# Kernel tuning notes

Hardware: AMD Instinct MI355X
Metric: run time of the kernel (lower is better)

## Reference

```python
import jax, jax.numpy as jnp
import numpy as np

N = 50000      # nodes (B-rep faces)
E = 800000     # directed edges (avg degree 16)
F_IN = 9       # 8 surface-type flags + is_feature
H1, H2, C = 512, 128, 2


def setup_inputs() -> dict:
    key = jax.random.key(0)
    ks = jax.random.split(key, 8)
    x = jax.random.normal(ks[0], (N, F_IN), dtype=jnp.float32)
    edge_index = jax.random.randint(ks[1], (2, E), 0, N, dtype=jnp.int64)
    W1 = jax.random.normal(ks[2], (F_IN, H1), dtype=jnp.float32) / np.sqrt(F_IN)
    b1 = jnp.zeros((H1,), dtype=jnp.float32)
    W2 = jax.random.normal(ks[3], (H1, H2), dtype=jnp.float32) / np.sqrt(H1)
    b2 = jnp.zeros((H2,), dtype=jnp.float32)
    W3 = jax.random.normal(ks[4], (H2, C), dtype=jnp.float32) / np.sqrt(H2)
    b3 = jnp.zeros((C,), dtype=jnp.float32)
    return {"x": x, "W1": W1, "b1": b1, "W2": W2, "b2": b2,
            "W3": W3, "b3": b3, "edge_index": edge_index}


def reference(x, W1, b1, W2, b2, W3, b3, edge_index):
    n = x.shape[0]
    self_idx = jnp.arange(n, dtype=edge_index.dtype)
    # GCN with self-loops and symmetric normalization (PyG gcn_norm)
    src = jnp.concatenate([edge_index[0], self_idx])  # [E+N]
    dst = jnp.concatenate([edge_index[1], self_idx])  # [E+N]
    deg = jax.ops.segment_sum(jnp.ones_like(src, dtype=x.dtype), dst, num_segments=n)
    dinv = jnp.where(deg > 0, jax.lax.rsqrt(jnp.maximum(deg, 1.0)), 0.0)
    norm = dinv[src] * dinv[dst]  # [E+N]

    def gcn(h, W, b):
        h = h @ W                                   # [N, out]
        msg = h[src] * norm[:, None]                # gather + scale
        return jax.ops.segment_sum(msg, dst, num_segments=n) + b  # scatter-add

    h = jax.nn.relu(gcn(x, W1, b1))
    h = jax.nn.relu(gcn(h, W2, b2))
    # F.dropout with training=False is identity (inference mode)
    h = gcn(h, W3, b3)
    return jax.nn.log_softmax(h, axis=1)
```

## Files before the change

kernel.cpp:

```cpp
#include <hip/hip_runtime.h>
#include <hip/hip_bf16.h>

typedef __attribute__((ext_vector_type(8))) short short8;
typedef __attribute__((ext_vector_type(4))) float float4v;
typedef unsigned int uint;

#define NBLK 192

static __device__ __forceinline__ float2 up_bf2(uint v) {
    float2 r;
    r.x = __uint_as_float(v << 16);
    r.y = __uint_as_float(v & 0xffff0000u);
    return r;
}
static __device__ __forceinline__ short f2bf_bits(float x) {
    union { __hip_bfloat16 h; short s; } u;
    u.h = __float2bfloat16(x);
    return u.s;
}


__global__ __launch_bounds__(256) void k_hist(const int* __restrict__ dst, int E, int chunk,
        int shift, int nbuck, int* __restrict__ histBlk) {
    __shared__ int h[256];
    h[threadIdx.x] = 0;
    __syncthreads();
    int blk = blockIdx.x;
    int e0 = blk * chunk, e1 = min(E, e0 + chunk);
    for (int e = e0 + threadIdx.x; e < e1; e += 256)
        atomicAdd(&h[dst[e] >> shift], 1);
    __syncthreads();
    if (threadIdx.x < nbuck) histBlk[threadIdx.x * NBLK + blk] = h[threadIdx.x];
}


__global__ __launch_bounds__(256) void k_btot(const int* __restrict__ histBlk,
                                              int* __restrict__ btot) {
    __shared__ int s[256];
    int b = blockIdx.x, t = threadIdx.x;
    s[t] = (t < NBLK) ? histBlk[b * NBLK + t] : 0;
    __syncthreads();
    for (int off = 128; off; off >>= 1) {
        if (t < off) s[t] += s[t + off];
        __syncthreads();
    }
    if (t == 0) btot[b] = s[0];
}


__global__ __launch_bounds__(256) void k_bscan(const int* __restrict__ histBlk,
        const int* __restrict__ btot, int nbuck,
        int* __restrict__ baseBlk, int* __restrict__ bucketBase) {
    __shared__ int s[256], sb[256];
    int b = blockIdx.x, t = threadIdx.x;
    int v = (t < NBLK) ? histBlk[b * NBLK + t] : 0;
    s[t] = v;
    sb[t] = (t < nbuck) ? btot[t] : 0;
    __syncthreads();
    for (int off = 1; off < 256; off <<= 1) {
        int u = (t >= off) ? s[t - off] : 0;
        int u2 = (t >= off) ? sb[t - off] : 0;
        __syncthreads();
        s[t] += u;
        sb[t] += u2;
        __syncthreads();
    }
    int base = (b > 0) ? sb[b - 1] : 0;
    if (t < NBLK) baseBlk[b * NBLK + t] = base + s[t] - v;
    if (t == 0) bucketBase[b] = base;
}


__global__ __launch_bounds__(256) void k_scatterbin(const int* __restrict__ src,
        const int* __restrict__ dst, int E, int chunk, int shift, int nbuck,
        const int* __restrict__ baseBlk, uint* __restrict__ binned) {
    __shared__ int cur[256];
    int blk = blockIdx.x;
    if (threadIdx.x < nbuck) cur[threadIdx.x] = baseBlk[threadIdx.x * NBLK + blk];
    __syncthreads();
    int e0 = blk * chunk, e1 = min(E, e0 + chunk);
    int mask = (1 << shift) - 1;
    for (int e = e0 + threadIdx.x; e < e1; e += 256) {
        int d = dst[e];
        int pos = atomicAdd(&cur[d >> shift], 1);
        binned[pos] = (uint)src[e] | ((uint)(d & mask) << 24);
    }
}


__global__ __launch_bounds__(256) void k_csrbuild(const uint* __restrict__ binned,
        const int* __restrict__ bucketBase, const float* __restrict__ x,
        int E, int shift, int n, int nbuck,
        int* __restrict__ row_ptr, float* __restrict__ dinv, float* __restrict__ xs,
        int* __restrict__ csr) {
    __shared__ int cnt[256], lcur[256];
    int b = blockIdx.x, t = threadIdx.x;
    cnt[t] = 0;
    __syncthreads();
    int lo = bucketBase[b];
    int hi = (b + 1 < nbuck) ? bucketBase[b + 1] : E;
    for (int e = lo + t; e < hi; e += 256)
        atomicAdd(&cnt[binned[e] >> 24], 1);
    __syncthreads();
    int c = cnt[t];
    lcur[t] = c;
    __syncthreads();
    for (int off = 1; off < 256; off <<= 1) {
        int u = (t >= off) ? lcur[t - off] : 0;
        __syncthreads();
        lcur[t] += u;
        __syncthreads();
    }
    int node0 = b << shift;
    int nodeEnd = min(n, (b + 1) << shift);
    int cntNodes = nodeEnd - node0;
    int myBase = lo + lcur[t] - c;
    if (t < cntNodes) {
        row_ptr[node0 + t] = myBase;
        dinv[node0 + t] = rsqrtf((float)(c + 1));
    }
    if (b == nbuck - 1 && t == 0) row_ptr[n] = E;
    for (int j = t; j < cntNodes * 9; j += 256) {
        int nl = j / 9, f = j - nl * 9;
        float dnl = rsqrtf((float)(cnt[nl] + 1));
        xs[(size_t)(node0 + nl) * 9 + f] = dnl * x[(size_t)(node0 + nl) * 9 + f];
    }
    __syncthreads();
    lcur[t] = myBase;
    __syncthreads();
    for (int e = lo + t; e < hi; e += 256) {
        uint p = binned[e];
        int pos = atomicAdd(&lcur[p >> 24], 1);
        csr[pos] = (int)(p & 0xFFFFFF);
    }
}


__global__ __launch_bounds__(256) void k_agg1(const float* __restrict__ xs,
                       const float* __restrict__ dinv,
                       const int* __restrict__ row_ptr, const int* __restrict__ csr,
                       float* __restrict__ aggx, int n) {
    int node = blockIdx.x * 16 + (threadIdx.x >> 4);
    if (node >= n) return;
    int f = threadIdx.x & 15;
    bool act = f < 9;
    float acc = act ? xs[node * 9 + f] : 0.f;
    int e0 = row_ptr[node], e1 = row_ptr[node + 1];
    int e = e0;
    for (; e + 4 <= e1; e += 4) {
        int s0 = csr[e], s1 = csr[e + 1], s2 = csr[e + 2], s3 = csr[e + 3];
        float x0 = act ? xs[s0 * 9 + f] : 0.f;
        float x1 = act ? xs[s1 * 9 + f] : 0.f;
        float x2 = act ? xs[s2 * 9 + f] : 0.f;
        float x3 = act ? xs[s3 * 9 + f] : 0.f;
        acc += (x0 + x1) + (x2 + x3);
    }
    for (; e < e1; ++e) {
        int sA = csr[e];
        acc += act ? xs[sA * 9 + f] : 0.f;
    }
    if (act) aggx[node * 9 + f] = dinv[node] * acc;
}

__global__ __launch_bounds__(256, 2) void k_l12(const float* __restrict__ aggx,
                       const float* __restrict__ W1, const float* __restrict__ b1,
                       const float* __restrict__ W2, const float* __restrict__ dinv,
                       __hip_bfloat16* __restrict__ t2, int n, int nchunk) {
    __shared__ short bsh[64 * 64 * 8];
    int t = threadIdx.x;
    int colbase = blockIdx.y << 6;

    for (int idx = t; idx < 64 * 64; idx += 256) {
        int kb = idx >> 6, c = idx & 63;
        const float* wp = W2 + (size_t)(kb * 8) * 128 + colbase + c;
        short8 o;
#pragma unroll
        for (int j = 0; j < 8; ++j) o[j] = f2bf_bits(wp[j * 128]);
        *reinterpret_cast<short8*>(bsh + (size_t)idx * 8) = o;
    }
    __syncthreads();

    int wid = t >> 6, lane = t & 63;
    int chunk = blockIdx.x * 4 + wid;
    if (chunk >= nchunk) return;
    int r = lane & 15, quad = lane >> 4;
    int m0 = chunk << 6;

    float av[4][9];
#pragma unroll
    for (int mt = 0; mt < 4; ++mt) {
        const float* ap = aggx + (size_t)(m0 + mt * 16 + r) * 9;
        float4 a0 = *(const float4*)ap;
        float4 a1 = *(const float4*)(ap + 4);
        av[mt][0] = a0.x; av[mt][1] = a0.y; av[mt][2] = a0.z; av[mt][3] = a0.w;
        av[mt][4] = a1.x; av[mt][5] = a1.y; av[mt][6] = a1.z; av[mt][7] = a1.w;
        av[mt][8] = ap[8];
    }

    float4v acc[4][4];
#pragma unroll
    for (int mt = 0; mt < 4; ++mt)
#pragma unroll
        for (int cg = 0; cg < 4; ++cg) acc[mt][cg] = (float4v){0, 0, 0, 0};

#pragma unroll
    for (int kt = 0; kt < 16; ++kt) {
        int kb = kt * 32 + quad * 8;
        float4 bb0 = *(const float4*)(b1 + kb);
        float4 bb1 = *(const float4*)(b1 + kb + 4);
        float a8[4][8];
#pragma unroll
        for (int mt = 0; mt < 4; ++mt) {
            a8[mt][0] = bb0.x; a8[mt][1] = bb0.y; a8[mt][2] = bb0.z; a8[mt][3] = bb0.w;
            a8[mt][4] = bb1.x; a8[mt][5] = bb1.y; a8[mt][6] = bb1.z; a8[mt][7] = bb1.w;
        }
#pragma unroll
        for (int f = 0; f < 9; ++f) {
            const float* wp = W1 + f * 512 + kb;
            float4 wa = *(const float4*)wp;
            float4 wb = *(const float4*)(wp + 4);
#pragma unroll
            for (int mt = 0; mt < 4; ++mt) {
                float x = av[mt][f];
                a8[mt][0] += x * wa.x; a8[mt][1] += x * wa.y;
                a8[mt][2] += x * wa.z; a8[mt][3] += x * wa.w;
                a8[mt][4] += x * wb.x; a8[mt][5] += x * wb.y;
                a8[mt][6] += x * wb.z; a8[mt][7] += x * wb.w;
            }
        }
        short8 afr[4];
#pragma unroll
        for (int mt = 0; mt < 4; ++mt)
#pragma unroll
            for (int j = 0; j < 8; ++j)
                afr[mt][j] = f2bf_bits(fmaxf(a8[mt][j], 0.f));

        short8 b[4];
#pragma unroll
        for (int cg = 0; cg < 4; ++cg)
            b[cg] = *reinterpret_cast<const short8*>(
                bsh + (size_t)(((kt * 4 + quad) * 64) + cg * 16 + r) * 8);
#pragma unroll
        for (int mt = 0; mt < 4; ++mt)
#pragma unroll
            for (int cg = 0; cg < 4; ++cg)
                acc[mt][cg] = __builtin_amdgcn_mfma_f32_16x16x32_bf16(afr[mt], b[cg], acc[mt][cg], 0, 0, 0);
    }

#pragma unroll
    for (int mt = 0; mt < 4; ++mt)
#pragma unroll
        for (int i = 0; i < 4; ++i) {
            int node = m0 + mt * 16 + quad * 4 + i;
            if (node < n) {
                float di = dinv[node];
                __hip_bfloat16* op = t2 + (size_t)node * 128 + colbase + r;
#pragma unroll
                for (int cg = 0; cg < 4; ++cg)
                    op[cg * 16] = __float2bfloat16(di * acc[mt][cg][i]);
            }
        }
}


__global__ __launch_bounds__(256) void k_agg2(const uint* __restrict__ t2u,
                       const float* __restrict__ dinv,
                       const int* __restrict__ row_ptr, const int* __restrict__ csr,
                       const float* __restrict__ b2, const float* __restrict__ W3,
                       float2* __restrict__ t3, int n) {
    int node = blockIdx.x * 4 + (threadIdx.x >> 6);
    if (node >= n) return;
    int lane = threadIdx.x & 63;
    float2 p = up_bf2(t2u[(size_t)node * 64 + lane]);
    float a0 = p.x, a1 = p.y;
    int e0 = row_ptr[node], e1 = row_ptr[node + 1];
    int e = e0;
    for (; e + 8 <= e1; e += 8) {
        int si[8];
        uint ri[8];
#pragma unroll
        for (int j = 0; j < 8; ++j) si[j] = csr[e + j];
#pragma unroll
        for (int j = 0; j < 8; ++j) ri[j] = t2u[(size_t)si[j] * 64 + lane];
#pragma unroll
        for (int j = 0; j < 8; ++j) {
            float2 q = up_bf2(ri[j]);
            a0 += q.x;
            a1 += q.y;
        }
    }
    for (; e + 2 <= e1; e += 2) {
        int s0 = csr[e], s1 = csr[e + 1];
        uint r0 = t2u[(size_t)s0 * 64 + lane];
        uint r1 = t2u[(size_t)s1 * 64 + lane];
        float2 q0 = up_bf2(r0), q1 = up_bf2(r1);
        a0 += q0.x + q1.x;
        a1 += q0.y + q1.y;
    }
    if (e < e1) {
        float2 q0 = up_bf2(t2u[(size_t)csr[e] * 64 + lane]);
        a0 += q0.x;
        a1 += q0.y;
    }
    float di = dinv[node];
    float2 bb = *reinterpret_cast<const float2*>(b2 + 2 * lane);
    float h0 = fmaxf(di * a0 + bb.x, 0.f);
    float h1v = fmaxf(di * a1 + bb.y, 0.f);
    float4 wv = *reinterpret_cast<const float4*>(W3 + 4 * lane);
    float c0 = h0 * wv.x + h1v * wv.z;
    float c1 = h0 * wv.y + h1v * wv.w;
#pragma unroll
    for (int off = 32; off; off >>= 1) {
        c0 += __shfl_xor(c0, off);
        c1 += __shfl_xor(c1, off);
    }
    if (lane == 0) t3[node] = make_float2(di * c0, di * c1);
}


__global__ void k_agg3(const float2* __restrict__ t3, const float* __restrict__ dinv,
                       const int* __restrict__ row_ptr, const int* __restrict__ csr,
                       const float* __restrict__ b3, float2* __restrict__ outv, int n) {
    int node = blockIdx.x * blockDim.x + threadIdx.x;
    if (node >= n) return;
    float2 s = t3[node];
    float a0 = s.x, a1 = s.y;
    int e0 = row_ptr[node], e1 = row_ptr[node + 1];
    int e = e0;
    for (; e + 4 <= e1; e += 4) {
        int s0 = csr[e], s1 = csr[e + 1], s2 = csr[e + 2], s3 = csr[e + 3];
        float2 q0 = t3[s0], q1 = t3[s1], q2 = t3[s2], q3 = t3[s3];
        a0 += q0.x + q1.x + q2.x + q3.x;
        a1 += q0.y + q1.y + q2.y + q3.y;
    }
    for (; e < e1; ++e) {
        float2 q0 = t3[csr[e]];
        a0 += q0.x;
        a1 += q0.y;
    }
    float di = dinv[node];
    float z0 = di * a0 + b3[0];
    float z1 = di * a1 + b3[1];
    float m = fmaxf(z0, z1);
    float lse = m + logf(expf(z0 - m) + expf(z1 - m));
    outv[node] = make_float2(z0 - lse, z1 - lse);
}


extern "C" void kernel_launch(void* const* d_in, const int* in_sizes, int n_in,
                              void* d_out, int out_size, void* d_ws, size_t ws_size,
                              hipStream_t stream) {
    const float* x  = (const float*)d_in[0];
    const float* W1 = (const float*)d_in[1];
    const float* b1 = (const float*)d_in[2];
    const float* W2 = (const float*)d_in[3];
    const float* b2 = (const float*)d_in[4];
    const float* W3 = (const float*)d_in[5];
    const float* b3 = (const float*)d_in[6];
    const int* edges = (const int*)d_in[7];

    int n = in_sizes[0] / 9;
    int E = in_sizes[7] / 2;
    const int* src = edges;
    const int* dst = edges + E;

    char* p = (char*)d_ws;
    auto alloc = [&](size_t bytes) {
        char* q = p;
        p += (bytes + 511) & ~(size_t)511;
        return q;
    };
    float* dinv       = (float*)alloc((size_t)n * 4);
    int*   row_ptr    = (int*)alloc((size_t)(n + 1) * 4);
    int*   csr        = (int*)alloc((size_t)E * 4);
    int*   histBlk    = (int*)alloc((size_t)256 * NBLK * 4);
    int*   baseBlk    = (int*)alloc((size_t)256 * NBLK * 4);
    int*   btot       = (int*)alloc(256 * 4);
    int*   bucketBase = (int*)alloc(256 * 4);
    uint*  binned     = (uint*)alloc((size_t)E * 4);
    float* xs         = (float*)alloc((size_t)n * 9 * 4);
    float* aggx       = (float*)alloc((size_t)(n + 64) * 9 * 4);
    __hip_bfloat16* t2 = (__hip_bfloat16*)alloc((size_t)n * 128 * 2);
    float2* t3 = (float2*)alloc((size_t)n * 8);

    const int B = 256;
    int shift = 8;
    int nbuck = ((n - 1) >> shift) + 1;
    int chunk = (E + NBLK - 1) / NBLK;

    k_hist<<<NBLK, B, 0, stream>>>(dst, E, chunk, shift, nbuck, histBlk);
    k_btot<<<nbuck, B, 0, stream>>>(histBlk, btot);
    k_bscan<<<nbuck, B, 0, stream>>>(histBlk, btot, nbuck, baseBlk, bucketBase);
    k_scatterbin<<<NBLK, B, 0, stream>>>(src, dst, E, chunk, shift, nbuck, baseBlk, binned);
    k_csrbuild<<<nbuck, B, 0, stream>>>(binned, bucketBase, x, E, shift, n, nbuck,
                                        row_ptr, dinv, xs, csr);

    k_agg1<<<(n + 15) / 16, B, 0, stream>>>(xs, dinv, row_ptr, csr, aggx, n);

    int nchunk = (n + 63) / 64;
    dim3 g2((nchunk + 3) / 4, 2);
    k_l12<<<g2, 256, 0, stream>>>(aggx, W1, b1, W2, dinv, t2, n, nchunk);
    k_agg2<<<(n + 3) / 4, 256, 0, stream>>>((const uint*)t2, dinv, row_ptr, csr, b2, W3, t3, n);

    k_agg3<<<(n + B - 1) / B, B, 0, stream>>>(t3, dinv, row_ptr, csr, b3, (float2*)d_out, n);
}
```

Measured before the change: 216.1 us.

## Retile fused layer1-2 GEMM to 16-row tiles covering all 128 output columns

After: 218.2 us. About the same (+1.0%).

```diff
diff --git a/kernel.cpp b/kernel.cpp
--- a/kernel.cpp
+++ b/kernel.cpp
@@ -162,17 +162,16 @@
     if (act) aggx[node * 9 + f] = dinv[node] * acc;
 }
 
-__global__ __launch_bounds__(256, 2) void k_l12(const float* __restrict__ aggx,
+__global__ __launch_bounds__(512, 2) void k_l12(const float* __restrict__ aggx,
                        const float* __restrict__ W1, const float* __restrict__ b1,
                        const float* __restrict__ W2, const float* __restrict__ dinv,
-                       __hip_bfloat16* __restrict__ t2, int n, int nchunk) {
-    __shared__ short bsh[64 * 64 * 8];
+                       __hip_bfloat16* __restrict__ t2, int n, int ntile) {
+    __shared__ short bsh[64 * 128 * 8];
     int t = threadIdx.x;
-    int colbase = blockIdx.y << 6;
-
-    for (int idx = t; idx < 64 * 64; idx += 256) {
-        int kb = idx >> 6, c = idx & 63;
-        const float* wp = W2 + (size_t)(kb * 8) * 128 + colbase + c;
+
+    for (int idx = t; idx < 64 * 128; idx += 512) {
+        int kb = idx >> 7, c = idx & 127;
+        const float* wp = W2 + (size_t)(kb * 8) * 128 + c;
         short8 o;
 #pragma unroll
         for (int j = 0; j < 8; ++j) o[j] = f2bf_bits(wp[j * 128]);
@@ -181,85 +180,58 @@
     __syncthreads();
 
     int wid = t >> 6, lane = t & 63;
-    int chunk = blockIdx.x * 4 + wid;
-    if (chunk >= nchunk) return;
+    int tile = blockIdx.x * 8 + wid;
+    if (tile >= ntile) return;
     int r = lane & 15, quad = lane >> 4;
-    int m0 = chunk << 6;
-
-    float av[4][9];
-#pragma unroll
-    for (int mt = 0; mt < 4; ++mt) {
-        const float* ap = aggx + (size_t)(m0 + mt * 16 + r) * 9;
-        float4 a0 = *(const float4*)ap;
-        float4 a1 = *(const float4*)(ap + 4);
-        av[mt][0] = a0.x; av[mt][1] = a0.y; av[mt][2] = a0.z; av[mt][3] = a0.w;
-        av[mt][4] = a1.x; av[mt][5] = a1.y; av[mt][6] = a1.z; av[mt][7] = a1.w;
-        av[mt][8] = ap[8];
-    }
-
-    float4v acc[4][4];
-#pragma unroll
-    for (int mt = 0; mt < 4; ++mt)
-#pragma unroll
-        for (int cg = 0; cg < 4; ++cg) acc[mt][cg] = (float4v){0, 0, 0, 0};
+    int m0 = tile << 4;
+
+    const float* ap = aggx + (size_t)(m0 + r) * 9;
+    float4 a0 = *(const float4*)ap;
+    float4 a1 = *(const float4*)(ap + 4);
+    float av[9] = {a0.x, a0.y, a0.z, a0.w, a1.x, a1.y, a1.z, a1.w, ap[8]};
+
+    float4v acc[8];
+#pragma unroll
+    for (int cg = 0; cg < 8; ++cg) acc[cg] = (float4v){0, 0, 0, 0};
 
 #pragma unroll
     for (int kt = 0; kt < 16; ++kt) {
         int kb = kt * 32 + quad * 8;
         float4 bb0 = *(const float4*)(b1 + kb);
         float4 bb1 = *(const float4*)(b1 + kb + 4);
-        float a8[4][8];
-#pragma unroll
-        for (int mt = 0; mt < 4; ++mt) {
-            a8[mt][0] = bb0.x; a8[mt][1] = bb0.y; a8[mt][2] = bb0.z; a8[mt][3] = bb0.w;
-            a8[mt][4] = bb1.x; a8[mt][5] = bb1.y; a8[mt][6] = bb1.z; a8[mt][7] = bb1.w;
-        }
+        float a8[8] = {bb0.x, bb0.y, bb0.z, bb0.w, bb1.x, bb1.y, bb1.z, bb1.w};
 #pragma unroll
         for (int f = 0; f < 9; ++f) {
             const float* wp = W1 + f * 512 + kb;
             float4 wa = *(const float4*)wp;
             float4 wb = *(const float4*)(wp + 4);
-#pragma unroll
-            for (int mt = 0; mt < 4; ++mt) {
-                float x = av[mt][f];
-                a8[mt][0] += x * wa.x; a8[mt][1] += x * wa.y;
-                a8[mt][2] += x * wa.z; a8[mt][3] += x * wa.w;
-                a8[mt][4] += x * wb.x; a8[mt][5] += x * wb.y;
-                a8[mt][6] += x * wb.z; a8[mt][7] += x * wb.w;
-            }
+            float xv = av[f];
+            a8[0] += xv * wa.x; a8[1] += xv * wa.y; a8[2] += xv * wa.z; a8[3] += xv * wa.w;
+            a8[4] += xv * wb.x; a8[5] += xv * wb.y; a8[6] += xv * wb.z; a8[7] += xv * wb.w;
         }
-        short8 afr[4];
-#pragma unroll
-        for (int mt = 0; mt < 4; ++mt)
-#pragma unroll
-            for (int j = 0; j < 8; ++j)
-                afr[mt][j] = f2bf_bits(fmaxf(a8[mt][j], 0.f));
-
-        short8 b[4];
-#pragma unroll
-        for (int cg = 0; cg < 4; ++cg)
-            b[cg] = *reinterpret_cast<const short8*>(
-                bsh + (size_t)(((kt * 4 + quad) * 64) + cg * 16 + r) * 8);
-#pragma unroll
-        for (int mt = 0; mt < 4; ++mt)
-#pragma unroll
-            for (int cg = 0; cg < 4; ++cg)
-                acc[mt][cg] = __builtin_amdgcn_mfma_f32_16x16x32_bf16(afr[mt], b[cg], acc[mt][cg], 0, 0, 0);
-    }
-
-#pragma unroll
-    for (int mt = 0; mt < 4; ++mt)
-#pragma unroll
-        for (int i = 0; i < 4; ++i) {
-            int node = m0 + mt * 16 + quad * 4 + i;
-            if (node < n) {
-                float di = dinv[node];
-                __hip_bfloat16* op = t2 + (size_t)node * 128 + colbase + r;
-#pragma unroll
-                for (int cg = 0; cg < 4; ++cg)
-                    op[cg * 16] = __float2bfloat16(di * acc[mt][cg][i]);
-            }
+        short8 afr;
+#pragma unroll
+        for (int j = 0; j < 8; ++j) afr[j] = f2bf_bits(fmaxf(a8[j], 0.f));
+
+#pragma unroll
+        for (int cg = 0; cg < 8; ++cg) {
+            short8 b = *reinterpret_cast<const short8*>(
+                bsh + (size_t)(((kt * 4 + quad) * 128) + cg * 16 + r) * 8);
+            acc[cg] = __builtin_amdgcn_mfma_f32_16x16x32_bf16(afr, b, acc[cg], 0, 0, 0);
         }
+    }
+
+#pragma unroll
+    for (int i = 0; i < 4; ++i) {
+        int node = m0 + quad * 4 + i;
+        if (node < n) {
+            float di = dinv[node];
+            __hip_bfloat16* op = t2 + (size_t)node * 128 + r;
+#pragma unroll
+            for (int cg = 0; cg < 8; ++cg)
+                op[cg * 16] = __float2bfloat16(di * acc[cg][i]);
+        }
+    }
 }
 
 
@@ -397,9 +369,8 @@
 
     k_agg1<<<(n + 15) / 16, B, 0, stream>>>(xs, dinv, row_ptr, csr, aggx, n);
 
-    int nchunk = (n + 63) / 64;
-    dim3 g2((nchunk + 3) / 4, 2);
-    k_l12<<<g2, 256, 0, stream>>>(aggx, W1, b1, W2, dinv, t2, n, nchunk);
+    int ntile = (n + 15) / 16;
+    k_l12<<<(ntile + 7) / 8, 512, 0, stream>>>(aggx, W1, b1, W2, dinv, t2, n, ntile);
     k_agg2<<<(n + 3) / 4, 256, 0, stream>>>((const uint*)t2, dinv, row_ptr, csr, b2, W3, t3, n);
 
     k_agg3<<<(n + B - 1) / B, B, 0, stream>>>(t3, dinv, row_ptr, csr, b3, (float2*)d_out, n);
```
